# Optimization experiments

Hardware: AMD Instinct MI355X
Metric: run time of the kernel (lower is better)

The kernel has to match this reference:

```python
import jax, jax.numpy as jnp
import numpy as np

N_SIN = 3
BN_EPS = 1e-5

def kan(x, W1, W2, B1, B2):
    # x: [B, din]; W1: [din, dout, H, 1+2*n_sin]; W2: [din, dout, 1, H]
    # B1: [din, dout, H]; B2: [din, dout, 1]
    omega = (2.0 ** jnp.arange(N_SIN)).astype(x.dtype)          # [n_sin]
    ox = x[..., None] * omega                                   # [B, din, n_sin]
    feats = jnp.concatenate([x[..., None], jnp.sin(ox), jnp.cos(ox)], axis=-1)  # [B, din, F]
    h = jnp.einsum('bif,ijhf->bijh', feats, W1) + B1            # [B, din, dout, H]
    h = jax.nn.silu(h)
    out = jnp.einsum('bijh,ijh->bij', h, W2[:, :, 0, :]) + B2[:, :, 0]  # [B, din, dout]
    return out.sum(axis=1)                                      # [B, dout]

def setup_inputs() -> dict:
    key = jax.random.key(0)
    ks = jax.random.split(key, 20)
    B, DIN, DH, DOUT, H = 128, 128, 256, 128, 32
    F = 1 + 2 * N_SIN
    def n(k, shape, s=0.1):
        return jax.random.normal(k, shape, dtype=jnp.float32) * s
    return {
        'x': jax.random.normal(ks[0], (B, DIN), dtype=jnp.float32),
        'fc1_W1': n(ks[1], (DIN, DH, H, F)), 'fc1_W2': n(ks[2], (DIN, DH, 1, H)),
        'fc1_B1': n(ks[3], (DIN, DH, H)),    'fc1_B2': n(ks[4], (DIN, DH, 1)),
        'fc2_W1': n(ks[5], (DH, DOUT, H, F)), 'fc2_W2': n(ks[6], (DH, DOUT, 1, H)),
        'fc2_B1': n(ks[7], (DH, DOUT, H)),    'fc2_B2': n(ks[8], (DH, DOUT, 1)),
        'sk_W1': n(ks[9], (DIN, DOUT, H, F)), 'sk_W2': n(ks[10], (DIN, DOUT, 1, H)),
        'sk_B1': n(ks[11], (DIN, DOUT, H)),   'sk_B2': n(ks[12], (DIN, DOUT, 1)),
        'g1_w': n(ks[13], (DOUT, DOUT)), 'g1_b': n(ks[14], (DOUT,)),
        'g2_w': n(ks[15], (DOUT, DOUT)), 'g2_b': n(ks[16], (DOUT,)),
        'bn_w': jnp.ones((DOUT,), jnp.float32), 'bn_b': jnp.zeros((DOUT,), jnp.float32),
    }

def reference(x, fc1_W1, fc1_W2, fc1_B1, fc1_B2,
              fc2_W1, fc2_W2, fc2_B1, fc2_B2,
              sk_W1, sk_W2, sk_B1, sk_B2,
              g1_w, g1_b, g2_w, g2_b, bn_w, bn_b):
    residual = kan(x, sk_W1, sk_W2, sk_B1, sk_B2)                # [B, DOUT]
    h = kan(x, fc1_W1, fc1_W2, fc1_B1, fc1_B2)                   # [B, DH]
    h = jax.nn.elu(h)
    h = kan(h, fc2_W1, fc2_W2, fc2_B1, fc2_B2)                   # [B, DOUT]
    # dropout: eval-mode identity
    sig = jax.nn.sigmoid(h @ g1_w.T + g1_b)
    h = sig * (h @ g2_w.T + g2_b)                                # GLU gate
    h = h + residual
    mean = h.mean(axis=0)
    var = h.var(axis=0)                                          # biased, as torch BN
    h = (h - mean) * jax.lax.rsqrt(var + BN_EPS) * bn_w + bn_b
    return h
```

## Files before the change

### kernel.cpp

```cpp
#include <hip/hip_runtime.h>
#include <cstddef>
#include <cstdint>

#define BATCH 128
#define NF 7

__device__ __forceinline__ float fast_silu(float a) {
    float e = __builtin_amdgcn_exp2f(a * -1.442695041f);
    return a * __builtin_amdgcn_rcpf(1.0f + e);
}

__global__ void feats_kernel(const float* __restrict__ in, float* __restrict__ out,
                             int din, int do_elu) {
    int t = blockIdx.x * blockDim.x + threadIdx.x;
    if (t >= din * BATCH) return;
    int b = t & (BATCH - 1);
    int i = t >> 7;
    float v = in[b * din + i];
    if (do_elu) v = (v > 0.0f) ? v : (__builtin_amdgcn_exp2f(v * 1.442695041f) - 1.0f);
    float s1, c1, s2, c2, s4, c4;
    sincosf(v, &s1, &c1);
    sincosf(2.0f * v, &s2, &c2);
    sincosf(4.0f * v, &s4, &c4);
    float* o = out + (size_t)i * (NF * BATCH) + b;
    o[0 * BATCH] = v;
    o[1 * BATCH] = s1;
    o[2 * BATCH] = s2;
    o[3 * BATCH] = s4;
    o[4 * BATCH] = c1;
    o[5 * BATCH] = c2;
    o[6 * BATCH] = c4;
}

template <int DIN, int DOUT, int CHUNK>
__global__ __launch_bounds__(256, 4) void kan_kernel(
    const float* __restrict__ fx,
    const float* __restrict__ W1,
    const float* __restrict__ W2,
    const float* __restrict__ B1,
    const float* __restrict__ B2,
    float* __restrict__ out)
{
    __shared__ float smem[4 * 320];
    __shared__ float redbuf[4 * 128];
    const int j    = blockIdx.x;
    const int tid  = threadIdx.x;
    const int w    = tid >> 6;
    const int lane = tid & 63;
    const int wb   = w * 320;
    const int i0   = blockIdx.y * CHUNK;

    float tot0 = 0.0f, tot1 = 0.0f;

    for (int t = 0; t < CHUNK / 4; ++t) {
        const int i = i0 + t * 4 + w;
        const float* w1p = W1 + ((size_t)i * DOUT + j) * 224;
        if (lane < 56) {
            const float4 v = *(const float4*)(w1p + lane * 4);
            const float* vp = (const float*)&v;
            #pragma unroll
            for (int q = 0; q < 4; ++q) {
                int e = lane * 4 + q;
                smem[wb + (e / 7) * 8 + (e % 7)] = vp[q];
            }
        }
        const float* b1p = B1 + ((size_t)i * DOUT + j) * 32;
        const float* w2p = W2 + ((size_t)i * DOUT + j) * 32;
        if (lane < 32) smem[wb + 256 + 2 * lane]              = b1p[lane];
        else           smem[wb + 256 + 2 * (lane - 32) + 1]   = w2p[lane - 32];
        __syncthreads();

        const float* fp = fx + (size_t)i * (NF * BATCH) + lane;
        float f0[NF], f1[NF];
        #pragma unroll
        for (int f = 0; f < NF; ++f) { f0[f] = fp[f * BATCH]; f1[f] = fp[f * BATCH + 64]; }

        float o0 = 0.0f, o1 = 0.0f;
        #pragma unroll 8
        for (int h = 0; h < 32; ++h) {
            float b1v = smem[wb + 256 + 2 * h];
            float w2v = smem[wb + 256 + 2 * h + 1];
            float a0 = b1v, a1 = b1v;
            #pragma unroll
            for (int f = 0; f < NF; ++f) {
                float ww = smem[wb + h * 8 + f];
                a0 = fmaf(f0[f], ww, a0);
                a1 = fmaf(f1[f], ww, a1);
            }
            o0 = fmaf(fast_silu(a0), w2v, o0);
            o1 = fmaf(fast_silu(a1), w2v, o1);
        }
        float b2v = B2[(size_t)i * DOUT + j];
        tot0 += o0 + b2v;
        tot1 += o1 + b2v;
        __syncthreads();
    }

    redbuf[w * 128 + lane]      = tot0;
    redbuf[w * 128 + 64 + lane] = tot1;
    __syncthreads();
    if (tid < 128) {
        float s = redbuf[tid] + redbuf[128 + tid] + redbuf[256 + tid] + redbuf[384 + tid];
        atomicAdd(&out[(size_t)tid * DOUT + j], s);
    }
}

__device__ __forceinline__ int shidx(int k, int b) { return (k << 7) + ((b + k) & 127); }

__global__ __launch_bounds__(128) void glu_bn_kernel(
    const float* __restrict__ h2,
    const float* __restrict__ resid,
    const float* __restrict__ g1w, const float* __restrict__ g1b,
    const float* __restrict__ g2w, const float* __restrict__ g2b,
    const float* __restrict__ bnw, const float* __restrict__ bnb,
    float* __restrict__ out)
{
    __shared__ float sh[128 * 128];
    const int j   = blockIdx.x;
    const int tid = threadIdx.x;

    for (int b2 = 0; b2 < 128; ++b2)
        sh[shidx(tid, b2)] = h2[(size_t)b2 * 128 + tid];
    __syncthreads();

    const float* g1r = g1w + (size_t)j * 128;
    const float* g2r = g2w + (size_t)j * 128;
    float d1 = g1b[j], d2 = g2b[j];
    for (int k = 0; k < 128; ++k) {
        float hv = sh[shidx(k, tid)];
        d1 = fmaf(hv, g1r[k], d1);
        d2 = fmaf(hv, g2r[k], d2);
    }
    float sg = __builtin_amdgcn_rcpf(1.0f + __builtin_amdgcn_exp2f(d1 * -1.442695041f));
    float v  = sg * d2 + resid[(size_t)tid * 128 + j];

    float s = v, ss = v * v;
    #pragma unroll
    for (int m = 1; m < 64; m <<= 1) {
        s  += __shfl_xor(s,  m, 64);
        ss += __shfl_xor(ss, m, 64);
    }
    __syncthreads();
    if ((tid & 63) == 0) { sh[(tid >> 6) * 2] = s; sh[(tid >> 6) * 2 + 1] = ss; }
    __syncthreads();
    s  = sh[0] + sh[2];
    ss = sh[1] + sh[3];
    float mean = s * (1.0f / 128.0f);
    float var  = ss * (1.0f / 128.0f) - mean * mean;
    out[(size_t)tid * 128 + j] = (v - mean) * rsqrtf(var + 1e-5f) * bnw[j] + bnb[j];
}

extern "C" void kernel_launch(void* const* d_in, const int* in_sizes, int n_in,
                              void* d_out, int out_size, void* d_ws, size_t ws_size,
                              hipStream_t stream) {
    const float* x      = (const float*)d_in[0];
    const float* fc1_W1 = (const float*)d_in[1];
    const float* fc1_W2 = (const float*)d_in[2];
    const float* fc1_B1 = (const float*)d_in[3];
    const float* fc1_B2 = (const float*)d_in[4];
    const float* fc2_W1 = (const float*)d_in[5];
    const float* fc2_W2 = (const float*)d_in[6];
    const float* fc2_B1 = (const float*)d_in[7];
    const float* fc2_B2 = (const float*)d_in[8];
    const float* sk_W1  = (const float*)d_in[9];
    const float* sk_W2  = (const float*)d_in[10];
    const float* sk_B1  = (const float*)d_in[11];
    const float* sk_B2  = (const float*)d_in[12];
    const float* g1w    = (const float*)d_in[13];
    const float* g1b    = (const float*)d_in[14];
    const float* g2w    = (const float*)d_in[15];
    const float* g2b    = (const float*)d_in[16];
    const float* bnw    = (const float*)d_in[17];
    const float* bnb    = (const float*)d_in[18];
    float* out = (float*)d_out;

    float* ws    = (float*)d_ws;
    float* h1    = ws;
    float* h2    = h1 + 128 * 256;
    float* resid = h2 + 128 * 128;
    float* fx    = resid + 128 * 128;
    float* fh    = fx + 128 * NF * 128;

    hipMemsetAsync(h1, 0, (size_t)(128 * 256 + 2 * 128 * 128) * sizeof(float), stream);

    feats_kernel<<<dim3((128 * BATCH) / 256), 256, 0, stream>>>(x, fx, 128, 0);

    kan_kernel<128, 256, 32><<<dim3(256, 4), 256, 0, stream>>>(
        fx, fc1_W1, fc1_W2, fc1_B1, fc1_B2, h1);
    kan_kernel<128, 128, 16><<<dim3(128, 8), 256, 0, stream>>>(
        fx, sk_W1, sk_W2, sk_B1, sk_B2, resid);

    feats_kernel<<<dim3((256 * BATCH) / 256), 256, 0, stream>>>(h1, fh, 256, 1);

    kan_kernel<256, 128, 32><<<dim3(128, 8), 256, 0, stream>>>(
        fh, fc2_W1, fc2_W2, fc2_B1, fc2_B2, h2);

    glu_bn_kernel<<<dim3(128), 128, 0, stream>>>(
        h2, resid, g1w, g1b, g2w, g2b, bnw, bnb, out);
}
```

Measured before the change: 174.7 us.

## Pack batch pairs into float2 FMAs, fold B1 into LDS rows, drop barriers

The feature buffer is re-laid out so each lane reads two interleaved batch values as a single float2. The hidden-unit loop then runs on 2-wide vector FMAs, which can map to packed FP32 instructions. B1 is stored in the unused eighth slot of each W1 row in LDS so each hidden unit's weights and bias come from two float4 LDS reads. The block-wide __syncthreads are removed because each wave only touches its own LDS region. Occupancy hint and chunk sizes are changed to launch more, smaller blocks, which adds more atomicAdd traffic in exchange.

```diff
diff --git a/kernel.cpp b/kernel.cpp
--- a/kernel.cpp
+++ b/kernel.cpp
@@ -5,9 +5,26 @@
 #define BATCH 128
 #define NF 7
 
-__device__ __forceinline__ float fast_silu(float a) {
-    float e = __builtin_amdgcn_exp2f(a * -1.442695041f);
-    return a * __builtin_amdgcn_rcpf(1.0f + e);
+typedef float v2f __attribute__((ext_vector_type(2)));
+
+__device__ __forceinline__ v2f vfma(v2f a, float b, v2f c) {
+#if __has_builtin(__builtin_elementwise_fma)
+    return __builtin_elementwise_fma(a, (v2f)(b), c);
+#else
+    v2f r; r.x = fmaf(a.x, b, c.x); r.y = fmaf(a.y, b, c.y); return r;
+#endif
+}
+
+__device__ __forceinline__ v2f silu2(v2f a) {
+    v2f t = a * -1.442695041f;
+    v2f e;
+    e.x = __builtin_amdgcn_exp2f(t.x);
+    e.y = __builtin_amdgcn_exp2f(t.y);
+    v2f d = e + 1.0f;
+    v2f r;
+    r.x = __builtin_amdgcn_rcpf(d.x);
+    r.y = __builtin_amdgcn_rcpf(d.y);
+    return a * r;
 }
 
 __global__ void feats_kernel(const float* __restrict__ in, float* __restrict__ out,
@@ -22,18 +39,18 @@
     sincosf(v, &s1, &c1);
     sincosf(2.0f * v, &s2, &c2);
     sincosf(4.0f * v, &s4, &c4);
-    float* o = out + (size_t)i * (NF * BATCH) + b;
-    o[0 * BATCH] = v;
-    o[1 * BATCH] = s1;
-    o[2 * BATCH] = s2;
-    o[3 * BATCH] = s4;
-    o[4 * BATCH] = c1;
-    o[5 * BATCH] = c2;
-    o[6 * BATCH] = c4;
+    float* o = out + (size_t)i * (NF * 128) + (b & 63) * 2 + (b >> 6);
+    o[0 * 128] = v;
+    o[1 * 128] = s1;
+    o[2 * 128] = s2;
+    o[3 * 128] = s4;
+    o[4 * 128] = c1;
+    o[5 * 128] = c2;
+    o[6 * 128] = c4;
 }
 
 template <int DIN, int DOUT, int CHUNK>
-__global__ __launch_bounds__(256, 4) void kan_kernel(
+__global__ __launch_bounds__(256, 8) void kan_kernel(
     const float* __restrict__ fx,
     const float* __restrict__ W1,
     const float* __restrict__ W2,
@@ -50,7 +67,7 @@
     const int wb   = w * 320;
     const int i0   = blockIdx.y * CHUNK;
 
-    float tot0 = 0.0f, tot1 = 0.0f;
+    v2f tot = (v2f)(0.0f);
 
     for (int t = 0; t < CHUNK / 4; ++t) {
         const int i = i0 + t * 4 + w;
@@ -66,38 +83,41 @@
         }
         const float* b1p = B1 + ((size_t)i * DOUT + j) * 32;
         const float* w2p = W2 + ((size_t)i * DOUT + j) * 32;
-        if (lane < 32) smem[wb + 256 + 2 * lane]              = b1p[lane];
-        else           smem[wb + 256 + 2 * (lane - 32) + 1]   = w2p[lane - 32];
-        __syncthreads();
-
-        const float* fp = fx + (size_t)i * (NF * BATCH) + lane;
-        float f0[NF], f1[NF];
+        if (lane < 32) smem[wb + lane * 8 + 7]       = b1p[lane];
+        else           smem[wb + 256 + (lane - 32)]  = w2p[lane - 32];
+
+        const float* fp = fx + (size_t)i * (NF * 128) + lane * 2;
+        v2f f[NF];
         #pragma unroll
-        for (int f = 0; f < NF; ++f) { f0[f] = fp[f * BATCH]; f1[f] = fp[f * BATCH + 64]; }
-
-        float o0 = 0.0f, o1 = 0.0f;
-        #pragma unroll 8
-        for (int h = 0; h < 32; ++h) {
-            float b1v = smem[wb + 256 + 2 * h];
-            float w2v = smem[wb + 256 + 2 * h + 1];
-            float a0 = b1v, a1 = b1v;
+        for (int ff = 0; ff < NF; ++ff) f[ff] = *(const v2f*)(fp + ff * 128);
+
+        v2f o = (v2f)(0.0f);
+        #pragma unroll 2
+        for (int h4 = 0; h4 < 8; ++h4) {
+            const float4 w2q = *(const float4*)&smem[wb + 256 + h4 * 4];
+            const float* w2s = (const float*)&w2q;
             #pragma unroll
-            for (int f = 0; f < NF; ++f) {
-                float ww = smem[wb + h * 8 + f];
-                a0 = fmaf(f0[f], ww, a0);
-                a1 = fmaf(f1[f], ww, a1);
+            for (int hh = 0; hh < 4; ++hh) {
+                const int h = h4 * 4 + hh;
+                const float4 L  = *(const float4*)&smem[wb + h * 8];
+                const float4 Hq = *(const float4*)&smem[wb + h * 8 + 4];
+                v2f a = (v2f)(Hq.w);
+                a = vfma(f[0], L.x,  a);
+                a = vfma(f[1], L.y,  a);
+                a = vfma(f[2], L.z,  a);
+                a = vfma(f[3], L.w,  a);
+                a = vfma(f[4], Hq.x, a);
+                a = vfma(f[5], Hq.y, a);
+                a = vfma(f[6], Hq.z, a);
+                o = vfma(silu2(a), w2s[hh], o);
             }
-            o0 = fmaf(fast_silu(a0), w2v, o0);
-            o1 = fmaf(fast_silu(a1), w2v, o1);
         }
         float b2v = B2[(size_t)i * DOUT + j];
-        tot0 += o0 + b2v;
-        tot1 += o1 + b2v;
-        __syncthreads();
-    }
-
-    redbuf[w * 128 + lane]      = tot0;
-    redbuf[w * 128 + 64 + lane] = tot1;
+        tot += o + b2v;
+    }
+
+    redbuf[w * 128 + lane]      = tot.x;
+    redbuf[w * 128 + 64 + lane] = tot.y;
     __syncthreads();
     if (tid < 128) {
         float s = redbuf[tid] + redbuf[128 + tid] + redbuf[256 + tid] + redbuf[384 + tid];
@@ -185,14 +205,14 @@
 
     feats_kernel<<<dim3((128 * BATCH) / 256), 256, 0, stream>>>(x, fx, 128, 0);
 
-    kan_kernel<128, 256, 32><<<dim3(256, 4), 256, 0, stream>>>(
+    kan_kernel<128, 256, 16><<<dim3(256, 8), 256, 0, stream>>>(
         fx, fc1_W1, fc1_W2, fc1_B1, fc1_B2, h1);
-    kan_kernel<128, 128, 16><<<dim3(128, 8), 256, 0, stream>>>(
+    kan_kernel<128, 128, 8><<<dim3(128, 16), 256, 0, stream>>>(
         fx, sk_W1, sk_W2, sk_B1, sk_B2, resid);
 
     feats_kernel<<<dim3((256 * BATCH) / 256), 256, 0, stream>>>(h1, fh, 256, 1);
 
-    kan_kernel<256, 128, 32><<<dim3(128, 8), 256, 0, stream>>>(
+    kan_kernel<256, 128, 16><<<dim3(128, 16), 256, 0, stream>>>(
         fh, fc2_W1, fc2_W2, fc2_B1, fc2_B2, h2);
 
     glu_bn_kernel<<<dim3(128), 128, 0, stream>>>(
```

Measured after the change: 160.3 us. 1.09x faster.

## Compute KAN first layer with bf16 MFMA and bf16 packed features

Applied to the files above, without the earlier changes.

Replaces the scalar FP32 feature-by-weight FMA loop with a 32x32x16 bf16 MFMA per (input, output, batch-tile). The bias is folded in as an eighth feature column fixed at one. Features are stored as packed bf16x8 per batch element, and weights are converted to bf16 on the fly, so the shared-memory staging and block barriers are gone. Each wave now handles its own input slice and reduces across half-waves with shuffles before the atomic adds. This trades precision (bf16 inputs) for matrix-core throughput, and half the lanes plus half of K sit idle as zero padding.

```diff
diff --git a/kernel.cpp b/kernel.cpp
--- a/kernel.cpp
+++ b/kernel.cpp
@@ -1,20 +1,29 @@
 #include <hip/hip_runtime.h>
+#include <hip/hip_bf16.h>
 #include <cstddef>
 #include <cstdint>
 
-#define BATCH 128
 #define NF 7
+
+typedef short bf16x8 __attribute__((ext_vector_type(8)));
+typedef float f32x16 __attribute__((ext_vector_type(16)));
+
+__device__ __forceinline__ unsigned short f2bf(float f) {
+    union { float f; unsigned u; } v; v.f = f;
+    unsigned r = v.u + 0x7fffu + ((v.u >> 16) & 1u);
+    return (unsigned short)(r >> 16);
+}
 
 __device__ __forceinline__ float fast_silu(float a) {
     float e = __builtin_amdgcn_exp2f(a * -1.442695041f);
     return a * __builtin_amdgcn_rcpf(1.0f + e);
 }
 
-__global__ void feats_kernel(const float* __restrict__ in, float* __restrict__ out,
+__global__ void feats_kernel(const float* __restrict__ in, unsigned short* __restrict__ out,
                              int din, int do_elu) {
     int t = blockIdx.x * blockDim.x + threadIdx.x;
-    if (t >= din * BATCH) return;
-    int b = t & (BATCH - 1);
+    if (t >= din * 128) return;
+    int b = t & 127;
     int i = t >> 7;
     float v = in[b * din + i];
     if (do_elu) v = (v > 0.0f) ? v : (__builtin_amdgcn_exp2f(v * 1.442695041f) - 1.0f);
@@ -22,86 +31,94 @@
     sincosf(v, &s1, &c1);
     sincosf(2.0f * v, &s2, &c2);
     sincosf(4.0f * v, &s4, &c4);
-    float* o = out + (size_t)i * (NF * BATCH) + b;
-    o[0 * BATCH] = v;
-    o[1 * BATCH] = s1;
-    o[2 * BATCH] = s2;
-    o[3 * BATCH] = s4;
-    o[4 * BATCH] = c1;
-    o[5 * BATCH] = c2;
-    o[6 * BATCH] = c4;
-}
-
-template <int DIN, int DOUT, int CHUNK>
-__global__ __launch_bounds__(256, 4) void kan_kernel(
-    const float* __restrict__ fx,
+    bf16x8 o;
+    o[0] = (short)f2bf(v);
+    o[1] = (short)f2bf(s1);
+    o[2] = (short)f2bf(s2);
+    o[3] = (short)f2bf(s4);
+    o[4] = (short)f2bf(c1);
+    o[5] = (short)f2bf(c2);
+    o[6] = (short)f2bf(c4);
+    o[7] = (short)0x3F80;
+    *(bf16x8*)(out + ((size_t)i * 128 + b) * 8) = o;
+}
+
+template <int DIN, int DOUT, int WCHUNK>
+__global__ __launch_bounds__(256, 4) void kan_mfma(
+    const unsigned short* __restrict__ fxb,
     const float* __restrict__ W1,
     const float* __restrict__ W2,
     const float* __restrict__ B1,
     const float* __restrict__ B2,
     float* __restrict__ out)
 {
-    __shared__ float smem[4 * 320];
-    __shared__ float redbuf[4 * 128];
     const int j    = blockIdx.x;
-    const int tid  = threadIdx.x;
-    const int w    = tid >> 6;
-    const int lane = tid & 63;
-    const int wb   = w * 320;
-    const int i0   = blockIdx.y * CHUNK;
-
-    float tot0 = 0.0f, tot1 = 0.0f;
-
-    for (int t = 0; t < CHUNK / 4; ++t) {
-        const int i = i0 + t * 4 + w;
-        const float* w1p = W1 + ((size_t)i * DOUT + j) * 224;
-        if (lane < 56) {
-            const float4 v = *(const float4*)(w1p + lane * 4);
-            const float* vp = (const float*)&v;
+    const int w    = threadIdx.x >> 6;
+    const int lane = threadIdx.x & 63;
+    const int hl   = lane & 31;
+    const int hi   = lane >> 5;
+    const int ib   = (blockIdx.y * 4 + w) * WCHUNK;
+
+    float acc0 = 0.f, acc1 = 0.f, acc2 = 0.f, acc3 = 0.f, b2acc = 0.f;
+
+    for (int t = 0; t < WCHUNK; ++t) {
+        const int i = ib + t;
+        const size_t task = (size_t)i * DOUT + j;
+
+        bf16x8 A = {0, 0, 0, 0, 0, 0, 0, 0};
+        if (hi == 0) {
+            const float* wr = W1 + task * 224 + (size_t)hl * 7;
+            float b1v = B1[task * 32 + hl];
+            A[0] = (short)f2bf(wr[0]);
+            A[1] = (short)f2bf(wr[1]);
+            A[2] = (short)f2bf(wr[2]);
+            A[3] = (short)f2bf(wr[3]);
+            A[4] = (short)f2bf(wr[4]);
+            A[5] = (short)f2bf(wr[5]);
+            A[6] = (short)f2bf(wr[6]);
+            A[7] = (short)f2bf(b1v);
+        }
+
+        const float* w2p = W2 + task * 32 + hi * 4;
+        const float4 w2a = *(const float4*)(w2p);
+        const float4 w2b = *(const float4*)(w2p + 8);
+        const float4 w2c = *(const float4*)(w2p + 16);
+        const float4 w2d = *(const float4*)(w2p + 24);
+        const float b2v = B2[task];
+
+        #pragma unroll
+        for (int bt = 0; bt < 4; ++bt) {
+            bf16x8 Bf = {0, 0, 0, 0, 0, 0, 0, 0};
+            if (hi == 0)
+                Bf = *(const bf16x8*)(fxb + ((size_t)i * 128 + bt * 32 + hl) * 8);
+            f32x16 Cz = {0.f,0.f,0.f,0.f,0.f,0.f,0.f,0.f,0.f,0.f,0.f,0.f,0.f,0.f,0.f,0.f};
+            f32x16 C = __builtin_amdgcn_mfma_f32_32x32x16_bf16(A, Bf, Cz, 0, 0, 0);
+            float bacc = 0.f;
             #pragma unroll
-            for (int q = 0; q < 4; ++q) {
-                int e = lane * 4 + q;
-                smem[wb + (e / 7) * 8 + (e % 7)] = vp[q];
+            for (int r = 0; r < 16; ++r) {
+                float wv = (r < 4)  ? ((const float*)&w2a)[r & 3]
+                         : (r < 8)  ? ((const float*)&w2b)[r & 3]
+                         : (r < 12) ? ((const float*)&w2c)[r & 3]
+                                    : ((const float*)&w2d)[r & 3];
+                bacc = fmaf(fast_silu(C[r]), wv, bacc);
             }
+            if (bt == 0) acc0 += bacc;
+            else if (bt == 1) acc1 += bacc;
+            else if (bt == 2) acc2 += bacc;
+            else acc3 += bacc;
         }
-        const float* b1p = B1 + ((size_t)i * DOUT + j) * 32;
-        const float* w2p = W2 + ((size_t)i * DOUT + j) * 32;
-        if (lane < 32) smem[wb + 256 + 2 * lane]              = b1p[lane];
-        else           smem[wb + 256 + 2 * (lane - 32) + 1]   = w2p[lane - 32];
-        __syncthreads();
-
-        const float* fp = fx + (size_t)i * (NF * BATCH) + lane;
-        float f0[NF], f1[NF];
-        #pragma unroll
-        for (int f = 0; f < NF; ++f) { f0[f] = fp[f * BATCH]; f1[f] = fp[f * BATCH + 64]; }
-
-        float o0 = 0.0f, o1 = 0.0f;
-        #pragma unroll 8
-        for (int h = 0; h < 32; ++h) {
-            float b1v = smem[wb + 256 + 2 * h];
-            float w2v = smem[wb + 256 + 2 * h + 1];
-            float a0 = b1v, a1 = b1v;
-            #pragma unroll
-            for (int f = 0; f < NF; ++f) {
-                float ww = smem[wb + h * 8 + f];
-                a0 = fmaf(f0[f], ww, a0);
-                a1 = fmaf(f1[f], ww, a1);
-            }
-            o0 = fmaf(fast_silu(a0), w2v, o0);
-            o1 = fmaf(fast_silu(a1), w2v, o1);
-        }
-        float b2v = B2[(size_t)i * DOUT + j];
-        tot0 += o0 + b2v;
-        tot1 += o1 + b2v;
-        __syncthreads();
-    }
-
-    redbuf[w * 128 + lane]      = tot0;
-    redbuf[w * 128 + 64 + lane] = tot1;
-    __syncthreads();
-    if (tid < 128) {
-        float s = redbuf[tid] + redbuf[128 + tid] + redbuf[256 + tid] + redbuf[384 + tid];
-        atomicAdd(&out[(size_t)tid * DOUT + j], s);
+        b2acc += b2v;
+    }
+
+    acc0 += __shfl_xor(acc0, 32);
+    acc1 += __shfl_xor(acc1, 32);
+    acc2 += __shfl_xor(acc2, 32);
+    acc3 += __shfl_xor(acc3, 32);
+    if (hi == 0) {
+        atomicAdd(&out[(size_t)(0 * 32 + hl) * DOUT + j], acc0 + b2acc);
+        atomicAdd(&out[(size_t)(1 * 32 + hl) * DOUT + j], acc1 + b2acc);
+        atomicAdd(&out[(size_t)(2 * 32 + hl) * DOUT + j], acc2 + b2acc);
+        atomicAdd(&out[(size_t)(3 * 32 + hl) * DOUT + j], acc3 + b2acc);
     }
 }
 
@@ -178,22 +195,22 @@
     float* h1    = ws;
     float* h2    = h1 + 128 * 256;
     float* resid = h2 + 128 * 128;
-    float* fx    = resid + 128 * 128;
-    float* fh    = fx + 128 * NF * 128;
+    unsigned short* fxb = (unsigned short*)(resid + 128 * 128);
+    unsigned short* fhb = fxb + 128 * 128 * 8;
 
     hipMemsetAsync(h1, 0, (size_t)(128 * 256 + 2 * 128 * 128) * sizeof(float), stream);
 
-    feats_kernel<<<dim3((128 * BATCH) / 256), 256, 0, stream>>>(x, fx, 128, 0);
-
-    kan_kernel<128, 256, 32><<<dim3(256, 4), 256, 0, stream>>>(
-        fx, fc1_W1, fc1_W2, fc1_B1, fc1_B2, h1);
-    kan_kernel<128, 128, 16><<<dim3(128, 8), 256, 0, stream>>>(
-        fx, sk_W1, sk_W2, sk_B1, sk_B2, resid);
-
-    feats_kernel<<<dim3((256 * BATCH) / 256), 256, 0, stream>>>(h1, fh, 256, 1);
-
-    kan_kernel<256, 128, 32><<<dim3(128, 8), 256, 0, stream>>>(
-        fh, fc2_W1, fc2_W2, fc2_B1, fc2_B2, h2);
+    feats_kernel<<<dim3(64), 256, 0, stream>>>(x, fxb, 128, 0);
+
+    kan_mfma<128, 256, 8><<<dim3(256, 4), 256, 0, stream>>>(
+        fxb, fc1_W1, fc1_W2, fc1_B1, fc1_B2, h1);
+    kan_mfma<128, 128, 8><<<dim3(128, 4), 256, 0, stream>>>(
+        fxb, sk_W1, sk_W2, sk_B1, sk_B2, resid);
+
+    feats_kernel<<<dim3(128), 256, 0, stream>>>(h1, fhb, 256, 1);
+
+    kan_mfma<256, 128, 8><<<dim3(128, 8), 256, 0, stream>>>(
+        fhb, fc2_W1, fc2_W2, fc2_B1, fc2_B2, h2);
 
     glu_bn_kernel<<<dim3(128), 128, 0, stream>>>(
         h2, resid, g1w, g1b, g2w, g2b, bnw, bnb, out);
```

Result: faster. 159.2 us (-8.9%).
